# Performance work log

Hardware: AMD Instinct MI355X
Metric: run time of the kernel (lower is better)

Reference implementation:

```python
import jax, jax.numpy as jnp
import numpy as np
import math

D_MODEL = 64
X_KS = 32   # input_kernel_size
Y_KS = 32   # output_kernel_size
HIDDEN = 256


def pos_enc(pos, d_model=D_MODEL):
    # standard interleaved sinusoidal encoding indexed by integer position
    i = jnp.arange(d_model // 2, dtype=jnp.float32)
    inv_freq = jnp.power(jnp.float32(10000.0), -(2.0 * i) / d_model)
    ang = pos.astype(jnp.float32)[:, None] * inv_freq[None, :]      # [N, d/2]
    pe = jnp.stack([jnp.sin(ang), jnp.cos(ang)], axis=-1)           # [N, d/2, 2]
    return pe.reshape(pos.shape[0], d_model)


def setup_inputs() -> dict:
    key = jax.random.key(0)
    ks = jax.random.split(key, 9)
    B, IN = 64, 1024
    d_in_w = 2 * D_MODEL + X_KS   # 160
    d_in_b = D_MODEL + Y_KS       # 96
    def lin(k, fan_in, fan_out):
        s = 1.0 / math.sqrt(fan_in)
        return jax.random.uniform(k, (fan_in, fan_out), jnp.float32, -s, s)
    return {
        "x": jax.random.normal(ks[0], (B, IN), jnp.float32),
        "output_size": 1024,
        "W1": lin(ks[1], d_in_w, HIDDEN), "b1": jnp.zeros((HIDDEN,), jnp.float32),
        "W2": lin(ks[2], HIDDEN, X_KS * Y_KS), "b2": jnp.zeros((X_KS * Y_KS,), jnp.float32),
        "Wb1": lin(ks[3], d_in_b, HIDDEN), "bb1": jnp.zeros((HIDDEN,), jnp.float32),
        "Wb2": lin(ks[4], HIDDEN, Y_KS), "bb2": jnp.zeros((Y_KS,), jnp.float32),
    }


def reference(x, output_size, W1, b1, W2, b2, Wb1, bb1, Wb2, bb2):
    B, input_size = x.shape
    gen_x = math.ceil(output_size / Y_KS)
    gen_y = math.ceil(input_size / X_KS)

    # pad x up to gen_y*X_KS and chunk into kernel windows, tiled gen_x times
    new_x = jnp.pad(x, ((0, 0), (0, gen_y * X_KS - input_size)))
    new_x = new_x.reshape(B, gen_y, X_KS)
    new_x = jnp.tile(new_x, (1, gen_x, 1))                          # [B, gx*gy, X_KS]

    arg_x = jnp.tile(jnp.arange(gen_x), gen_y)                      # [gx*gy]
    arg_y = jnp.repeat(jnp.arange(gen_y), gen_x)                    # [gx*gy]
    pe_x = jnp.broadcast_to(pos_enc(arg_x)[None], (B, gen_x * gen_y, D_MODEL))
    pe_y = jnp.broadcast_to(pos_enc(arg_y)[None], (B, gen_x * gen_y, D_MODEL))

    argument = jnp.concatenate([pe_x, pe_y, new_x], axis=2)         # [B, G, 2d+X_KS]

    # hypernetwork generates per-sample weight matrix
    h = jnp.tanh(argument @ W1 + b1)
    w = h @ W2 + b2                                                 # [B, G, X_KS*Y_KS]
    weight = w.reshape(B, gen_y * X_KS, gen_x * Y_KS)[:, :input_size, :output_size]

    out = jnp.einsum("bi,bio->bo", x, weight)                       # [B, output_size]

    # bias hypernetwork
    out_pad = jnp.pad(out, ((0, 0), (0, gen_x * Y_KS - output_size)))
    out_pad = out_pad.reshape(B, gen_x, Y_KS)
    pe_b = jnp.broadcast_to(pos_enc(jnp.arange(gen_x))[None], (B, gen_x, D_MODEL))
    hb = jnp.tanh(jnp.concatenate([out_pad, pe_b], axis=2) @ Wb1 + bb1)
    bias = (hb @ Wb2 + bb2).reshape(B, -1)[:, :output_size]

    return out + bias
```

## Files before the change

kernel.cpp:

```cpp
#include <hip/hip_runtime.h>
#include <math.h>

constexpr int B    = 64;
constexpr int IN   = 1024;
constexpr int OUTN = 1024;
constexpr int H    = 256;

#define LN10000 9.210340371976184f
#define TWO_LOG2E 2.8853900817779268f

__device__ __forceinline__ float fast_tanh(float x) {
    x = fminf(fmaxf(x, -15.0f), 15.0f);
    float e = __builtin_amdgcn_exp2f(x * TWO_LOG2E);
    return 1.0f - 2.0f * __builtin_amdgcn_rcpf(e + 1.0f);
}

__global__ void __launch_bounds__(256) k0_tables(const float* __restrict__ W1,
                                                 const float* __restrict__ b1,
                                                 float* __restrict__ PA,
                                                 float* __restrict__ PY) {
    __shared__ float pe[64];
    const int blk = blockIdx.x, tid = threadIdx.x;
    const int p = blk & 31, table = blk >> 5;
    if (tid < 32) {
        float freq = expf(-(2.0f * (float)tid / 64.0f) * LN10000);
        float a = (float)p * freq;
        pe[2 * tid]     = sinf(a);
        pe[2 * tid + 1] = cosf(a);
    }
    __syncthreads();
    const float* src = (table == 0) ? W1 : (W1 + 64 * H);
    float acc = (table == 0) ? b1[tid] : 0.0f;
    #pragma unroll 16
    for (int d = 0; d < 64; ++d) acc += pe[d] * src[d * H + tid];
    float* dst = (table == 0) ? PA : PY;
    dst[p * H + tid] = acc;
}

__global__ void __launch_bounds__(1024, 4) k1_v(const float* __restrict__ x,
                                                const float* __restrict__ W1,
                                                const float* __restrict__ PA,
                                                const float* __restrict__ PY,
                                                float* __restrict__ v,
                                                float* __restrict__ S) {
    __shared__ float As[2048];
    __shared__ float red[1024];
    __shared__ float sred[16];
    const int blk = blockIdx.x, tid = threadIdx.x;
    const int b = blk >> 2, cq = blk & 3, c0 = cq * 64;
    const int cl = tid & 63, jg = tid >> 6;
    const int p0 = jg * 2;

    const float xr = x[b * IN + tid];
    float w1reg[32];
    #pragma unroll
    for (int k = 0; k < 32; ++k) w1reg[k] = W1[(128 + k) * H + c0 + cl];
    float acc0 = PA[p0 * H + c0 + cl];
    float acc1 = PA[(p0 + 1) * H + c0 + cl];
    const float py0 = PY[p0 * H + c0 + cl];
    const float py1 = PY[(p0 + 1) * H + c0 + cl];

    if (cq == 0) {
        float s = xr;
        #pragma unroll
        for (int off = 32; off > 0; off >>= 1) s += __shfl_xor(s, off, 64);
        if (cl == 0) sred[jg] = s;
    }

    #pragma unroll
    for (int k = 0; k < 32; ++k) acc0 += __shfl(xr, k, 64) * w1reg[k];
    #pragma unroll
    for (int k = 0; k < 32; ++k) acc1 += __shfl(xr, 32 + k, 64) * w1reg[k];

    As[p0 * 64 + cl]       = acc0;
    As[(p0 + 1) * 64 + cl] = acc1;
    __syncthreads();

    if (cq == 0 && tid == 0) {
        float s = 0.0f;
        #pragma unroll
        for (int g = 0; g < 16; ++g) s += sred[g];
        S[b] = s;
    }

    float acc = 0.0f;
    #pragma unroll
    for (int jx = 0; jx < 32; ++jx) {
        const float a = As[jx * 64 + cl];
        acc += __shfl(xr, jx, 64)      * fast_tanh(a + py0);
        acc += __shfl(xr, 32 + jx, 64) * fast_tanh(a + py1);
    }
    red[tid] = acc;
    __syncthreads();
    if (tid < 64) {
        float s = 0.0f;
        #pragma unroll
        for (int g = 0; g < 16; ++g) s += red[g * 64 + tid];
        v[b * H + c0 + tid] = s;
    }
}

__global__ void __launch_bounds__(1024) k2_out(const float* __restrict__ v,
                                               const float* __restrict__ S,
                                               const float* __restrict__ W2,
                                               const float* __restrict__ b2,
                                               const float* __restrict__ Wb1,
                                               const float* __restrict__ bb1,
                                               const float* __restrict__ Wb2,
                                               const float* __restrict__ bb2,
                                               float* __restrict__ out) {
    __shared__ float vsh[2048];
    __shared__ float hpe[256];
    __shared__ float osp[1024];
    __shared__ float os[256];
    __shared__ float hbs[2048];
    __shared__ float bp[1024];
    __shared__ float Ssh[8];
    const int blk = blockIdx.x, tid = threadIdx.x;
    const int og = blk & 31, bg = blk >> 5, b0 = bg * 8;
    const int h = tid >> 8, u = tid & 255, bl = u >> 5, ol = u & 31;

    ((float2*)vsh)[tid] = ((const float2*)(v + b0 * H))[tid];
    if (tid < 8) Ssh[tid] = S[b0 + tid];
    if (tid < 256) {
        const int L = tid & 63;
        float freq = expf(-(2.0f * (float)(L >> 1) / 64.0f) * LN10000);
        float a = (float)og * freq;
        float pel = (L & 1) ? cosf(a) : sinf(a);
        float accp = bb1[tid];
        #pragma unroll 16
        for (int d = 0; d < 64; ++d)
            accp += __shfl(pel, d, 64) * Wb1[(32 + d) * H + tid];
        hpe[tid] = accp;
    }
    __syncthreads();

    const int o = og * 32 + ol;
    {
        float acc = (h == 0) ? Ssh[bl] * b2[o] : 0.0f;
        const float4* vr = (const float4*)(vsh + bl * H + h * 64);
        #pragma unroll
        for (int c4 = 0; c4 < 16; ++c4) {
            float4 v4 = vr[c4];
            const int c = h * 64 + c4 * 4;
            acc += v4.x * W2[(c + 0) * OUTN + o];
            acc += v4.y * W2[(c + 1) * OUTN + o];
            acc += v4.z * W2[(c + 2) * OUTN + o];
            acc += v4.w * W2[(c + 3) * OUTN + o];
        }
        osp[h * 256 + u] = acc;
    }
    __syncthreads();
    if (tid < 256)
        os[tid] = osp[tid] + osp[256 + tid] + osp[512 + tid] + osp[768 + tid];
    __syncthreads();
    {
        float a0 = hpe[h * 64 + ol];
        float a1 = hpe[h * 64 + 32 + ol];
        const float4* osr = (const float4*)(os + bl * 32);
        #pragma unroll
        for (int k4 = 0; k4 < 8; ++k4) {
            float4 o4 = osr[k4];
            const float* wr = Wb1 + (k4 * 4) * H + h * 64 + ol;
            a0 += o4.x * wr[0];         a1 += o4.x * wr[32];
            a0 += o4.y * wr[H];         a1 += o4.y * wr[H + 32];
            a0 += o4.z * wr[2 * H];     a1 += o4.z * wr[2 * H + 32];
            a0 += o4.w * wr[3 * H];     a1 += o4.w * wr[3 * H + 32];
        }
        hbs[bl * H + h * 64 + ol]      = fast_tanh(a0);
        hbs[bl * H + h * 64 + 32 + ol] = fast_tanh(a1);
    }
    __syncthreads();
    {
        float bias = (h == 0) ? bb2[ol] : 0.0f;
        const float4* hr = (const float4*)(hbs + bl * H + h * 64);
        #pragma unroll
        for (int c4 = 0; c4 < 16; ++c4) {
            float4 h4 = hr[c4];
            const int c = h * 64 + c4 * 4;
            bias += h4.x * Wb2[(c + 0) * 32 + ol];
            bias += h4.y * Wb2[(c + 1) * 32 + ol];
            bias += h4.z * Wb2[(c + 2) * 32 + ol];
            bias += h4.w * Wb2[(c + 3) * 32 + ol];
        }
        bp[h * 256 + u] = bias;
    }
    __syncthreads();
    if (tid < 256) {
        out[(b0 + (tid >> 5)) * OUTN + og * 32 + (tid & 31)] =
            os[tid] + bp[tid] + bp[256 + tid] + bp[512 + tid] + bp[768 + tid];
    }
}

extern "C" void kernel_launch(void* const* d_in, const int* in_sizes, int n_in,
                              void* d_out, int out_size, void* d_ws, size_t ws_size,
                              hipStream_t stream) {
    const float* x   = (const float*)d_in[0];
    const float* W1  = (const float*)d_in[2];
    const float* b1  = (const float*)d_in[3];
    const float* W2  = (const float*)d_in[4];
    const float* b2  = (const float*)d_in[5];
    const float* Wb1 = (const float*)d_in[6];
    const float* bb1 = (const float*)d_in[7];
    const float* Wb2 = (const float*)d_in[8];
    const float* bb2 = (const float*)d_in[9];
    float* out = (float*)d_out;

    float* v  = (float*)d_ws;
    float* S  = v + B * H;
    float* PA = S + B;
    float* PY = PA + 32 * H;

    hipLaunchKernelGGL(k0_tables, dim3(64),    dim3(256),  0, stream, W1, b1, PA, PY);
    hipLaunchKernelGGL(k1_v,      dim3(B * 4), dim3(1024), 0, stream, x, W1, PA, PY, v, S);
    hipLaunchKernelGGL(k2_out,    dim3(256),   dim3(1024), 0, stream,
                       v, S, W2, b2, Wb1, bb1, Wb2, bb2, out);
}
```

Before: 92.88 us.

## Fuse three kernels into one cooperative kernel with grid syncs

Merges the table, v-reduction and output kernels into a single cooperative launch of 256 blocks, using grid.sync between stages. Table precomputation now also covers the bias-PE hidden projection (HPE), and Wb2 is staged in shared memory. The x-dependent W1 partial product is computed before the first grid sync so it overlaps table construction. The aim is to remove inter-kernel launch gaps, at the cost of grid-wide barrier overhead and a union shared-memory footprint that may limit occupancy. It falls back to three separate launches if the cooperative launch fails.

```diff
diff --git a/kernel.cpp b/kernel.cpp
--- a/kernel.cpp
+++ b/kernel.cpp
@@ -1,5 +1,8 @@
 #include <hip/hip_runtime.h>
+#include <hip/hip_cooperative_groups.h>
 #include <math.h>
+
+namespace cg = cooperative_groups;
 
 constexpr int B    = 64;
 constexpr int IN   = 1024;
@@ -15,130 +18,153 @@
     return 1.0f - 2.0f * __builtin_amdgcn_rcpf(e + 1.0f);
 }
 
-__global__ void __launch_bounds__(256) k0_tables(const float* __restrict__ W1,
-                                                 const float* __restrict__ b1,
-                                                 float* __restrict__ PA,
-                                                 float* __restrict__ PY) {
-    __shared__ float pe[64];
-    const int blk = blockIdx.x, tid = threadIdx.x;
-    const int p = blk & 31, table = blk >> 5;
-    if (tid < 32) {
-        float freq = expf(-(2.0f * (float)tid / 64.0f) * LN10000);
-        float a = (float)p * freq;
-        pe[2 * tid]     = sinf(a);
-        pe[2 * tid + 1] = cosf(a);
-    }
-    __syncthreads();
-    const float* src = (table == 0) ? W1 : (W1 + 64 * H);
-    float acc = (table == 0) ? b1[tid] : 0.0f;
+struct SmemA {
+    float xs[1024];
+    float w1s[2048];
+    float As[2048];
+    float red[1024];
+};
+struct SmemB {
+    float vsh[2048];
+    float hpe[256];
+    float osp[1024];
+    float os[256];
+    float hbs[2048];
+    float Wb2s[8192];
+    float bp[1024];
+    float Ssh[8];
+};
+union Smem { SmemA a; SmemB b; };
+
+__device__ __forceinline__ void tables_body(int bid, int tid,
+                                            const float* __restrict__ W1,
+                                            const float* __restrict__ b1,
+                                            const float* __restrict__ Wb1,
+                                            const float* __restrict__ bb1,
+                                            float* __restrict__ PA,
+                                            float* __restrict__ PY,
+                                            float* __restrict__ HPE) {
+    const int idx = bid * 1024 + tid;
+    const int table = idx >> 13;
+    const int p = (idx >> 8) & 31, c = idx & 255;
+    const int L = tid & 63;
+    float freq = expf(-(2.0f * (float)(L >> 1) / 64.0f) * LN10000);
+    float a = (float)p * freq;
+    float pel = (L & 1) ? cosf(a) : sinf(a);
+    const float* src; float acc; float* dst;
+    if (table == 0)      { src = W1;           acc = b1[c];  dst = PA;  }
+    else if (table == 1) { src = W1 + 64 * H;  acc = 0.0f;   dst = PY;  }
+    else                 { src = Wb1 + 32 * H; acc = bb1[c]; dst = HPE; }
     #pragma unroll 16
-    for (int d = 0; d < 64; ++d) acc += pe[d] * src[d * H + tid];
-    float* dst = (table == 0) ? PA : PY;
-    dst[p * H + tid] = acc;
-}
-
-__global__ void __launch_bounds__(1024, 4) k1_v(const float* __restrict__ x,
-                                                const float* __restrict__ W1,
-                                                const float* __restrict__ PA,
-                                                const float* __restrict__ PY,
-                                                float* __restrict__ v,
-                                                float* __restrict__ S) {
-    __shared__ float As[2048];
-    __shared__ float red[1024];
-    __shared__ float sred[16];
-    const int blk = blockIdx.x, tid = threadIdx.x;
-    const int b = blk >> 2, cq = blk & 3, c0 = cq * 64;
-    const int cl = tid & 63, jg = tid >> 6;
-    const int p0 = jg * 2;
-
-    const float xr = x[b * IN + tid];
-    float w1reg[32];
+    for (int d = 0; d < 64; ++d)
+        acc += __shfl(pel, d, 64) * src[d * H + c];
+    dst[p * H + c] = acc;
+}
+
+__device__ __forceinline__ void k1_prefix(int bid, int tid,
+                                          const float* __restrict__ x,
+                                          const float* __restrict__ W1,
+                                          SmemA& sa, float& acc0, float& acc1,
+                                          float* __restrict__ S) {
+    const int b = bid >> 2, cq = bid & 3, c0 = cq * 64;
+    const int cl = tid & 63, jg = tid >> 6, p0 = jg * 2;
+
+    sa.xs[tid] = x[b * IN + tid];
     #pragma unroll
-    for (int k = 0; k < 32; ++k) w1reg[k] = W1[(128 + k) * H + c0 + cl];
-    float acc0 = PA[p0 * H + c0 + cl];
-    float acc1 = PA[(p0 + 1) * H + c0 + cl];
+    for (int i = 0; i < 2; ++i) {
+        const int idx = i * 1024 + tid;
+        const int p = idx >> 6, c = idx & 63;
+        sa.w1s[idx] = W1[(128 + p) * H + c0 + c];
+    }
+    __syncthreads();
+
+    if (cq == 0 && tid < 64) {
+        float s = 0.0f;
+        #pragma unroll
+        for (int i = 0; i < 16; ++i) s += sa.xs[tid + i * 64];
+        #pragma unroll
+        for (int off = 32; off > 0; off >>= 1) s += __shfl_xor(s, off, 64);
+        if (tid == 0) S[b] = s;
+    }
+
+    acc0 = 0.0f; acc1 = 0.0f;
+    #pragma unroll 8
+    for (int k = 0; k < 32; ++k) {
+        const float w = sa.w1s[k * 64 + cl];
+        acc0 += sa.xs[p0 * 32 + k] * w;
+        acc1 += sa.xs[(p0 + 1) * 32 + k] * w;
+    }
+}
+
+__device__ __forceinline__ void k1_finish(int bid, int tid,
+                                          const float* __restrict__ PA,
+                                          const float* __restrict__ PY,
+                                          SmemA& sa, float acc0, float acc1,
+                                          float* __restrict__ v) {
+    const int b = bid >> 2, cq = bid & 3, c0 = cq * 64;
+    const int cl = tid & 63, jg = tid >> 6, p0 = jg * 2;
+
+    acc0 += PA[p0 * H + c0 + cl];
+    acc1 += PA[(p0 + 1) * H + c0 + cl];
     const float py0 = PY[p0 * H + c0 + cl];
     const float py1 = PY[(p0 + 1) * H + c0 + cl];
-
-    if (cq == 0) {
-        float s = xr;
-        #pragma unroll
-        for (int off = 32; off > 0; off >>= 1) s += __shfl_xor(s, off, 64);
-        if (cl == 0) sred[jg] = s;
-    }
-
+    sa.As[p0 * 64 + cl]       = acc0;
+    sa.As[(p0 + 1) * 64 + cl] = acc1;
+    __syncthreads();
+
+    float Areg[32];
     #pragma unroll
-    for (int k = 0; k < 32; ++k) acc0 += __shfl(xr, k, 64) * w1reg[k];
-    #pragma unroll
-    for (int k = 0; k < 32; ++k) acc1 += __shfl(xr, 32 + k, 64) * w1reg[k];
-
-    As[p0 * 64 + cl]       = acc0;
-    As[(p0 + 1) * 64 + cl] = acc1;
-    __syncthreads();
-
-    if (cq == 0 && tid == 0) {
-        float s = 0.0f;
-        #pragma unroll
-        for (int g = 0; g < 16; ++g) s += sred[g];
-        S[b] = s;
-    }
-
+    for (int jx = 0; jx < 32; ++jx) Areg[jx] = sa.As[jx * 64 + cl];
     float acc = 0.0f;
     #pragma unroll
-    for (int jx = 0; jx < 32; ++jx) {
-        const float a = As[jx * 64 + cl];
-        acc += __shfl(xr, jx, 64)      * fast_tanh(a + py0);
-        acc += __shfl(xr, 32 + jx, 64) * fast_tanh(a + py1);
-    }
-    red[tid] = acc;
+    for (int r = 0; r < 2; ++r) {
+        const int jy = p0 + r;
+        const float pyv = r ? py1 : py0;
+        const float4* xr = (const float4*)(sa.xs + jy * 32);
+        #pragma unroll
+        for (int q8 = 0; q8 < 8; ++q8) {
+            float4 xv = xr[q8];
+            acc += xv.x * fast_tanh(Areg[q8 * 4 + 0] + pyv);
+            acc += xv.y * fast_tanh(Areg[q8 * 4 + 1] + pyv);
+            acc += xv.z * fast_tanh(Areg[q8 * 4 + 2] + pyv);
+            acc += xv.w * fast_tanh(Areg[q8 * 4 + 3] + pyv);
+        }
+    }
+    sa.red[tid] = acc;
     __syncthreads();
     if (tid < 64) {
         float s = 0.0f;
         #pragma unroll
-        for (int g = 0; g < 16; ++g) s += red[g * 64 + tid];
+        for (int g = 0; g < 16; ++g) s += sa.red[g * 64 + tid];
         v[b * H + c0 + tid] = s;
     }
 }
 
-__global__ void __launch_bounds__(1024) k2_out(const float* __restrict__ v,
-                                               const float* __restrict__ S,
-                                               const float* __restrict__ W2,
-                                               const float* __restrict__ b2,
-                                               const float* __restrict__ Wb1,
-                                               const float* __restrict__ bb1,
-                                               const float* __restrict__ Wb2,
-                                               const float* __restrict__ bb2,
-                                               float* __restrict__ out) {
-    __shared__ float vsh[2048];
-    __shared__ float hpe[256];
-    __shared__ float osp[1024];
-    __shared__ float os[256];
-    __shared__ float hbs[2048];
-    __shared__ float bp[1024];
-    __shared__ float Ssh[8];
-    const int blk = blockIdx.x, tid = threadIdx.x;
-    const int og = blk & 31, bg = blk >> 5, b0 = bg * 8;
+__device__ __forceinline__ void k2_body(int bid, int tid,
+                                        const float* __restrict__ v,
+                                        const float* __restrict__ S,
+                                        const float* __restrict__ W2,
+                                        const float* __restrict__ b2,
+                                        const float* __restrict__ Wb1,
+                                        const float* __restrict__ HPE,
+                                        const float* __restrict__ Wb2,
+                                        const float* __restrict__ bb2,
+                                        SmemB& sb, float* __restrict__ out) {
+    const int og = bid & 31, bg = bid >> 5, b0 = bg * 8;
     const int h = tid >> 8, u = tid & 255, bl = u >> 5, ol = u & 31;
 
-    ((float2*)vsh)[tid] = ((const float2*)(v + b0 * H))[tid];
-    if (tid < 8) Ssh[tid] = S[b0 + tid];
-    if (tid < 256) {
-        const int L = tid & 63;
-        float freq = expf(-(2.0f * (float)(L >> 1) / 64.0f) * LN10000);
-        float a = (float)og * freq;
-        float pel = (L & 1) ? cosf(a) : sinf(a);
-        float accp = bb1[tid];
-        #pragma unroll 16
-        for (int d = 0; d < 64; ++d)
-            accp += __shfl(pel, d, 64) * Wb1[(32 + d) * H + tid];
-        hpe[tid] = accp;
-    }
+    ((float2*)sb.vsh)[tid] = ((const float2*)(v + b0 * H))[tid];
+    #pragma unroll
+    for (int i = 0; i < 2; ++i)
+        ((float4*)sb.Wb2s)[i * 1024 + tid] = ((const float4*)Wb2)[i * 1024 + tid];
+    if (tid < 256) sb.hpe[tid] = HPE[og * H + tid];
+    if (tid < 8) sb.Ssh[tid] = S[b0 + tid];
     __syncthreads();
 
     const int o = og * 32 + ol;
     {
-        float acc = (h == 0) ? Ssh[bl] * b2[o] : 0.0f;
-        const float4* vr = (const float4*)(vsh + bl * H + h * 64);
+        float acc = (h == 0) ? sb.Ssh[bl] * b2[o] : 0.0f;
+        const float4* vr = (const float4*)(sb.vsh + bl * H + h * 64);
         #pragma unroll
         for (int c4 = 0; c4 < 16; ++c4) {
             float4 v4 = vr[c4];
@@ -148,16 +174,16 @@
             acc += v4.z * W2[(c + 2) * OUTN + o];
             acc += v4.w * W2[(c + 3) * OUTN + o];
         }
-        osp[h * 256 + u] = acc;
+        sb.osp[h * 256 + u] = acc;
     }
     __syncthreads();
     if (tid < 256)
-        os[tid] = osp[tid] + osp[256 + tid] + osp[512 + tid] + osp[768 + tid];
+        sb.os[tid] = sb.osp[tid] + sb.osp[256 + tid] + sb.osp[512 + tid] + sb.osp[768 + tid];
     __syncthreads();
     {
-        float a0 = hpe[h * 64 + ol];
-        float a1 = hpe[h * 64 + 32 + ol];
-        const float4* osr = (const float4*)(os + bl * 32);
+        float a0 = sb.hpe[h * 64 + ol];
+        float a1 = sb.hpe[h * 64 + 32 + ol];
+        const float4* osr = (const float4*)(sb.os + bl * 32);
         #pragma unroll
         for (int k4 = 0; k4 < 8; ++k4) {
             float4 o4 = osr[k4];
@@ -167,29 +193,90 @@
             a0 += o4.z * wr[2 * H];     a1 += o4.z * wr[2 * H + 32];
             a0 += o4.w * wr[3 * H];     a1 += o4.w * wr[3 * H + 32];
         }
-        hbs[bl * H + h * 64 + ol]      = fast_tanh(a0);
-        hbs[bl * H + h * 64 + 32 + ol] = fast_tanh(a1);
+        sb.hbs[bl * H + h * 64 + ol]      = fast_tanh(a0);
+        sb.hbs[bl * H + h * 64 + 32 + ol] = fast_tanh(a1);
     }
     __syncthreads();
     {
         float bias = (h == 0) ? bb2[ol] : 0.0f;
-        const float4* hr = (const float4*)(hbs + bl * H + h * 64);
+        const float4* hr = (const float4*)(sb.hbs + bl * H + h * 64);
         #pragma unroll
         for (int c4 = 0; c4 < 16; ++c4) {
             float4 h4 = hr[c4];
             const int c = h * 64 + c4 * 4;
-            bias += h4.x * Wb2[(c + 0) * 32 + ol];
-            bias += h4.y * Wb2[(c + 1) * 32 + ol];
-            bias += h4.z * Wb2[(c + 2) * 32 + ol];
-            bias += h4.w * Wb2[(c + 3) * 32 + ol];
+            bias += h4.x * sb.Wb2s[(c + 0) * 32 + ol];
+            bias += h4.y * sb.Wb2s[(c + 1) * 32 + ol];
+            bias += h4.z * sb.Wb2s[(c + 2) * 32 + ol];
+            bias += h4.w * sb.Wb2s[(c + 3) * 32 + ol];
         }
-        bp[h * 256 + u] = bias;
+        sb.bp[h * 256 + u] = bias;
     }
     __syncthreads();
     if (tid < 256) {
         out[(b0 + (tid >> 5)) * OUTN + og * 32 + (tid & 31)] =
-            os[tid] + bp[tid] + bp[256 + tid] + bp[512 + tid] + bp[768 + tid];
-    }
+            sb.os[tid] + sb.bp[tid] + sb.bp[256 + tid] + sb.bp[512 + tid] + sb.bp[768 + tid];
+    }
+}
+
+__global__ void __launch_bounds__(1024, 4)
+fused_all(const float* __restrict__ x,  const float* __restrict__ W1,
+          const float* __restrict__ b1, const float* __restrict__ W2,
+          const float* __restrict__ b2, const float* __restrict__ Wb1,
+          const float* __restrict__ bb1,const float* __restrict__ Wb2,
+          const float* __restrict__ bb2,float* __restrict__ out,
+          float* __restrict__ v, float* __restrict__ S,
+          float* __restrict__ PA, float* __restrict__ PY, float* __restrict__ HPE) {
+    __shared__ Smem sm;
+    const int bid = blockIdx.x, tid = threadIdx.x;
+    cg::grid_group grid = cg::this_grid();
+
+    if (bid < 24) tables_body(bid, tid, W1, b1, Wb1, bb1, PA, PY, HPE);
+
+    float acc0, acc1;
+    k1_prefix(bid, tid, x, W1, sm.a, acc0, acc1, S);
+
+    grid.sync();
+
+    k1_finish(bid, tid, PA, PY, sm.a, acc0, acc1, v);
+
+    grid.sync();
+
+    k2_body(bid, tid, v, S, W2, b2, Wb1, HPE, Wb2, bb2, sm.b, out);
+}
+
+__global__ void __launch_bounds__(1024) k0_t(const float* __restrict__ W1,
+                                             const float* __restrict__ b1,
+                                             const float* __restrict__ Wb1,
+                                             const float* __restrict__ bb1,
+                                             float* __restrict__ PA,
+                                             float* __restrict__ PY,
+                                             float* __restrict__ HPE) {
+    tables_body(blockIdx.x, threadIdx.x, W1, b1, Wb1, bb1, PA, PY, HPE);
+}
+
+__global__ void __launch_bounds__(1024, 4) k1_s(const float* __restrict__ x,
+                                                const float* __restrict__ W1,
+                                                const float* __restrict__ PA,
+                                                const float* __restrict__ PY,
+                                                float* __restrict__ v,
+                                                float* __restrict__ S) {
+    __shared__ SmemA sa;
+    float acc0, acc1;
+    k1_prefix(blockIdx.x, threadIdx.x, x, W1, sa, acc0, acc1, S);
+    k1_finish(blockIdx.x, threadIdx.x, PA, PY, sa, acc0, acc1, v);
+}
+
+__global__ void __launch_bounds__(1024) k2_s(const float* __restrict__ v,
+                                             const float* __restrict__ S,
+                                             const float* __restrict__ W2,
+                                             const float* __restrict__ b2,
+                                             const float* __restrict__ Wb1,
+                                             const float* __restrict__ HPE,
+                                             const float* __restrict__ Wb2,
+                                             const float* __restrict__ bb2,
+                                             float* __restrict__ out) {
+    __shared__ SmemB sb;
+    k2_body(blockIdx.x, threadIdx.x, v, S, W2, b2, Wb1, HPE, Wb2, bb2, sb, out);
 }
 
 extern "C" void kernel_launch(void* const* d_in, const int* in_sizes, int n_in,
@@ -206,13 +293,25 @@
     const float* bb2 = (const float*)d_in[9];
     float* out = (float*)d_out;
 
-    float* v  = (float*)d_ws;
-    float* S  = v + B * H;
-    float* PA = S + B;
-    float* PY = PA + 32 * H;
-
-    hipLaunchKernelGGL(k0_tables, dim3(64),    dim3(256),  0, stream, W1, b1, PA, PY);
-    hipLaunchKernelGGL(k1_v,      dim3(B * 4), dim3(1024), 0, stream, x, W1, PA, PY, v, S);
-    hipLaunchKernelGGL(k2_out,    dim3(256),   dim3(1024), 0, stream,
-                       v, S, W2, b2, Wb1, bb1, Wb2, bb2, out);
-}
+    float* v   = (float*)d_ws;
+    float* S   = v + B * H;
+    float* PA  = S + B;
+    float* PY  = PA + 32 * H;
+    float* HPE = PY + 32 * H;
+
+    void* args[] = { (void*)&x, (void*)&W1, (void*)&b1, (void*)&W2, (void*)&b2,
+                     (void*)&Wb1, (void*)&bb1, (void*)&Wb2, (void*)&bb2,
+                     (void*)&out, (void*)&v, (void*)&S,
+                     (void*)&PA, (void*)&PY, (void*)&HPE };
+    hipError_t e = hipLaunchCooperativeKernel((const void*)fused_all,
+                                              dim3(256), dim3(1024),
+                                              args, 0, stream);
+    if (e != hipSuccess) {
+        hipLaunchKernelGGL(k0_t, dim3(24),    dim3(1024), 0, stream,
+                           W1, b1, Wb1, bb1, PA, PY, HPE);
+        hipLaunchKernelGGL(k1_s, dim3(B * 4), dim3(1024), 0, stream,
+                           x, W1, PA, PY, v, S);
+        hipLaunchKernelGGL(k2_s, dim3(256),   dim3(1024), 0, stream,
+                           v, S, W2, b2, Wb1, HPE, Wb2, bb2, out);
+    }
+}
```

After: 156.4 us. 68.4% more time.

## Precompute bias PE table, stage x/W1 and Wb2 in LDS instead of shuffles

Applied to the files above, without the earlier changes.

The positional-encoding projection for the bias hypernetwork moves into the table kernel, which now runs 96 blocks, so k2 no longer recomputes sin/cos and a 64-step matvec in each of its 256 blocks. In k1, x and the W1 slice are staged in shared memory and read as float4 broadcasts instead of through per-element lane shuffles. The A values are held in registers, and the separate row-sum reduction is simplified. k2 copies the 32 KB Wb2 into LDS per block, which raises LDS use and may cut occupancy in exchange for cheaper strided reads.

```diff
diff --git a/kernel.cpp b/kernel.cpp
--- a/kernel.cpp
+++ b/kernel.cpp
@@ -17,8 +17,11 @@
 
 __global__ void __launch_bounds__(256) k0_tables(const float* __restrict__ W1,
                                                  const float* __restrict__ b1,
+                                                 const float* __restrict__ Wb1,
+                                                 const float* __restrict__ bb1,
                                                  float* __restrict__ PA,
-                                                 float* __restrict__ PY) {
+                                                 float* __restrict__ PY,
+                                                 float* __restrict__ HPE) {
     __shared__ float pe[64];
     const int blk = blockIdx.x, tid = threadIdx.x;
     const int p = blk & 31, table = blk >> 5;
@@ -29,11 +32,12 @@
         pe[2 * tid + 1] = cosf(a);
     }
     __syncthreads();
-    const float* src = (table == 0) ? W1 : (W1 + 64 * H);
-    float acc = (table == 0) ? b1[tid] : 0.0f;
+    const float* src; float acc; float* dst;
+    if (table == 0)      { src = W1;           acc = b1[tid];  dst = PA;  }
+    else if (table == 1) { src = W1 + 64 * H;  acc = 0.0f;     dst = PY;  }
+    else                 { src = Wb1 + 32 * H; acc = bb1[tid]; dst = HPE; }
     #pragma unroll 16
     for (int d = 0; d < 64; ++d) acc += pe[d] * src[d * H + tid];
-    float* dst = (table == 0) ? PA : PY;
     dst[p * H + tid] = acc;
 }
 
@@ -43,52 +47,72 @@
                                                 const float* __restrict__ PY,
                                                 float* __restrict__ v,
                                                 float* __restrict__ S) {
+    __shared__ float xs[1024];
+    __shared__ float w1s[2048];
     __shared__ float As[2048];
     __shared__ float red[1024];
-    __shared__ float sred[16];
     const int blk = blockIdx.x, tid = threadIdx.x;
     const int b = blk >> 2, cq = blk & 3, c0 = cq * 64;
-    const int cl = tid & 63, jg = tid >> 6;
-    const int p0 = jg * 2;
-
-    const float xr = x[b * IN + tid];
-    float w1reg[32];
-    #pragma unroll
-    for (int k = 0; k < 32; ++k) w1reg[k] = W1[(128 + k) * H + c0 + cl];
+    const int cl = tid & 63, jg = tid >> 6, p0 = jg * 2;
+
+    xs[tid] = x[b * IN + tid];
+    #pragma unroll
+    for (int i = 0; i < 2; ++i) {
+        const int idx = i * 1024 + tid;
+        const int p = idx >> 6, c = idx & 63;
+        w1s[idx] = W1[(128 + p) * H + c0 + c];
+    }
     float acc0 = PA[p0 * H + c0 + cl];
     float acc1 = PA[(p0 + 1) * H + c0 + cl];
     const float py0 = PY[p0 * H + c0 + cl];
     const float py1 = PY[(p0 + 1) * H + c0 + cl];
-
-    if (cq == 0) {
-        float s = xr;
+    __syncthreads();
+
+    if (cq == 0 && tid < 64) {
+        float s = 0.0f;
+        #pragma unroll
+        for (int i = 0; i < 16; ++i) s += xs[tid + i * 64];
         #pragma unroll
         for (int off = 32; off > 0; off >>= 1) s += __shfl_xor(s, off, 64);
-        if (cl == 0) sred[jg] = s;
-    }
-
-    #pragma unroll
-    for (int k = 0; k < 32; ++k) acc0 += __shfl(xr, k, 64) * w1reg[k];
-    #pragma unroll
-    for (int k = 0; k < 32; ++k) acc1 += __shfl(xr, 32 + k, 64) * w1reg[k];
-
+        if (tid == 0) S[b] = s;
+    }
+
+    {
+        const float4* x0 = (const float4*)(xs + p0 * 32);
+        const float4* x1 = (const float4*)(xs + (p0 + 1) * 32);
+        #pragma unroll
+        for (int q8 = 0; q8 < 8; ++q8) {
+            float4 a4 = x0[q8], b4 = x1[q8];
+            const float w0 = w1s[(q8 * 4 + 0) * 64 + cl];
+            const float w1 = w1s[(q8 * 4 + 1) * 64 + cl];
+            const float w2 = w1s[(q8 * 4 + 2) * 64 + cl];
+            const float w3 = w1s[(q8 * 4 + 3) * 64 + cl];
+            acc0 += a4.x * w0; acc1 += b4.x * w0;
+            acc0 += a4.y * w1; acc1 += b4.y * w1;
+            acc0 += a4.z * w2; acc1 += b4.z * w2;
+            acc0 += a4.w * w3; acc1 += b4.w * w3;
+        }
+    }
     As[p0 * 64 + cl]       = acc0;
     As[(p0 + 1) * 64 + cl] = acc1;
     __syncthreads();
 
-    if (cq == 0 && tid == 0) {
-        float s = 0.0f;
-        #pragma unroll
-        for (int g = 0; g < 16; ++g) s += sred[g];
-        S[b] = s;
-    }
-
+    float Areg[32];
+    #pragma unroll
+    for (int jx = 0; jx < 32; ++jx) Areg[jx] = As[jx * 64 + cl];
     float acc = 0.0f;
     #pragma unroll
-    for (int jx = 0; jx < 32; ++jx) {
-        const float a = As[jx * 64 + cl];
-        acc += __shfl(xr, jx, 64)      * fast_tanh(a + py0);
-        acc += __shfl(xr, 32 + jx, 64) * fast_tanh(a + py1);
+    for (int r = 0; r < 2; ++r) {
+        const float pyv = r ? py1 : py0;
+        const float4* xr = (const float4*)(xs + (p0 + r) * 32);
+        #pragma unroll
+        for (int q8 = 0; q8 < 8; ++q8) {
+            float4 xv = xr[q8];
+            acc += xv.x * fast_tanh(Areg[q8 * 4 + 0] + pyv);
+            acc += xv.y * fast_tanh(Areg[q8 * 4 + 1] + pyv);
+            acc += xv.z * fast_tanh(Areg[q8 * 4 + 2] + pyv);
+            acc += xv.w * fast_tanh(Areg[q8 * 4 + 3] + pyv);
+        }
     }
     red[tid] = acc;
     __syncthreads();
@@ -105,7 +129,7 @@
                                                const float* __restrict__ W2,
                                                const float* __restrict__ b2,
                                                const float* __restrict__ Wb1,
-                                               const float* __restrict__ bb1,
+                                               const float* __restrict__ HPE,
                                                const float* __restrict__ Wb2,
                                                const float* __restrict__ bb2,
                                                float* __restrict__ out) {
@@ -114,6 +138,7 @@
     __shared__ float osp[1024];
     __shared__ float os[256];
     __shared__ float hbs[2048];
+    __shared__ float Wb2s[8192];
     __shared__ float bp[1024];
     __shared__ float Ssh[8];
     const int blk = blockIdx.x, tid = threadIdx.x;
@@ -121,18 +146,11 @@
     const int h = tid >> 8, u = tid & 255, bl = u >> 5, ol = u & 31;
 
     ((float2*)vsh)[tid] = ((const float2*)(v + b0 * H))[tid];
+    #pragma unroll
+    for (int i = 0; i < 2; ++i)
+        ((float4*)Wb2s)[i * 1024 + tid] = ((const float4*)Wb2)[i * 1024 + tid];
+    if (tid < 256) hpe[tid] = HPE[og * H + tid];
     if (tid < 8) Ssh[tid] = S[b0 + tid];
-    if (tid < 256) {
-        const int L = tid & 63;
-        float freq = expf(-(2.0f * (float)(L >> 1) / 64.0f) * LN10000);
-        float a = (float)og * freq;
-        float pel = (L & 1) ? cosf(a) : sinf(a);
-        float accp = bb1[tid];
-        #pragma unroll 16
-        for (int d = 0; d < 64; ++d)
-            accp += __shfl(pel, d, 64) * Wb1[(32 + d) * H + tid];
-        hpe[tid] = accp;
-    }
     __syncthreads();
 
     const int o = og * 32 + ol;
@@ -178,10 +196,10 @@
         for (int c4 = 0; c4 < 16; ++c4) {
             float4 h4 = hr[c4];
             const int c = h * 64 + c4 * 4;
-            bias += h4.x * Wb2[(c + 0) * 32 + ol];
-            bias += h4.y * Wb2[(c + 1) * 32 + ol];
-            bias += h4.z * Wb2[(c + 2) * 32 + ol];
-            bias += h4.w * Wb2[(c + 3) * 32 + ol];
+            bias += h4.x * Wb2s[(c + 0) * 32 + ol];
+            bias += h4.y * Wb2s[(c + 1) * 32 + ol];
+            bias += h4.z * Wb2s[(c + 2) * 32 + ol];
+            bias += h4.w * Wb2s[(c + 3) * 32 + ol];
         }
         bp[h * 256 + u] = bias;
     }
@@ -206,13 +224,16 @@
     const float* bb2 = (const float*)d_in[9];
     float* out = (float*)d_out;
 
-    float* v  = (float*)d_ws;
-    float* S  = v + B * H;
-    float* PA = S + B;
-    float* PY = PA + 32 * H;
-
-    hipLaunchKernelGGL(k0_tables, dim3(64),    dim3(256),  0, stream, W1, b1, PA, PY);
-    hipLaunchKernelGGL(k1_v,      dim3(B * 4), dim3(1024), 0, stream, x, W1, PA, PY, v, S);
+    float* v   = (float*)d_ws;
+    float* S   = v + B * H;
+    float* PA  = S + B;
+    float* PY  = PA + 32 * H;
+    float* HPE = PY + 32 * H;
+
+    hipLaunchKernelGGL(k0_tables, dim3(96),    dim3(256),  0, stream,
+                       W1, b1, Wb1, bb1, PA, PY, HPE);
+    hipLaunchKernelGGL(k1_v,      dim3(B * 4), dim3(1024), 0, stream,
+                       x, W1, PA, PY, v, S);
     hipLaunchKernelGGL(k2_out,    dim3(256),   dim3(1024), 0, stream,
-                       v, S, W2, b2, Wb1, bb1, Wb2, bb2, out);
-}
+                       v, S, W2, b2, Wb1, HPE, Wb2, bb2, out);
+}
```

New measurement: 89.56 us (median of 2 runs). -3.6%, faster.
